# Performance work log

Measured on AMD Instinct MI355X. Metric: run time of the kernel, lower is better.

The kernel has to match this reference:

```python
import jax, jax.numpy as jnp
import numpy as np

D_MODEL = 32
KEY_CH = 32
HEADS = 4
BIAS = 0.1


def setup_inputs() -> dict:
    key = jax.random.key(0)
    ks = jax.random.split(key, 8)
    Nu, Ni, d = 8192, 8192, D_MODEL
    s = 1.0 / np.sqrt(d)
    return {
        "user_embeddings": jax.random.normal(ks[0], (Nu, d), jnp.float32),
        "item_embeddings": jax.random.normal(ks[1], (Ni, d), jnp.float32),
        "keys_w": jax.random.uniform(ks[2], (d, KEY_CH), jnp.float32, -s, s),
        "keys_b": jax.random.uniform(ks[3], (KEY_CH,), jnp.float32, -s, s),
        "queries_w": jax.random.uniform(ks[4], (d, KEY_CH), jnp.float32, -s, s),
        "queries_b": jax.random.uniform(ks[5], (KEY_CH,), jnp.float32, -s, s),
        "reproj_w": jax.random.uniform(ks[6], (KEY_CH * HEADS, KEY_CH), jnp.float32, -s, s),
        "reproj_b": jax.random.uniform(ks[7], (KEY_CH,), jnp.float32, -s, s),
    }


def reference(user_embeddings, item_embeddings, keys_w, keys_b,
              queries_w, queries_b, reproj_w, reproj_b):
    Nu, d = user_embeddings.shape
    Ni = item_embeddings.shape[0]
    hk = KEY_CH // HEADS  # per-head key channels = 8
    keys = user_embeddings @ keys_w + keys_b          # [Nu, 32]
    queries = item_embeddings @ queries_w + queries_b  # [Ni, 32]
    # split into heads: [N, H, hk]
    k = jax.nn.softmax(keys.reshape(Nu, HEADS, hk), axis=0)      # softmax over users (dim 0)
    q = jax.nn.softmax(queries.reshape(Ni, HEADS, hk), axis=2)   # softmax over features (dim 1)
    # context per head: relu(key @ query^T - 0.1) -> [H, Nu, Ni]
    ctx = jax.nn.relu(jnp.einsum('uhk,ihk->hui', k, q) - BIAS)
    # attended = context^T @ user_embeddings -> [Ni, H, d]
    att = jnp.einsum('hui,ud->ihd', ctx, user_embeddings)
    agg = att.reshape(Ni, HEADS * d)  # concat heads along dim 1 (head-major, matches torch.cat)
    proj = agg @ reproj_w + reproj_b  # [Ni, 32]
    # dropout is identity in eval mode; residual add
    return item_embeddings + proj
```

## Files before the change

kernel.cpp:

```cpp
#include <hip/hip_runtime.h>

#define NU 8192
#define NI 8192
#define DM 32
#define KC 32
#define HEADS 4
#define HK 8
#define BIASV 0.1f

#define UBLK 128

__global__ __launch_bounds__(256) void k_embed(
    const float* __restrict__ U, const float* __restrict__ I,
    const float* __restrict__ Wk, const float* __restrict__ bk,
    const float* __restrict__ Wq, const float* __restrict__ bq,
    float* __restrict__ keys, float* __restrict__ q,
    float* __restrict__ part_s, float* __restrict__ part_m)
{
    __shared__ float Ws[DM * KC];
    __shared__ float bs[KC];
    __shared__ float wps[4][HEADS][HK];
    __shared__ float wpm[4][HEADS][HK];

    const int blk = blockIdx.x;
    const int t   = threadIdx.x;
    const int g   = blk * 256 + t;
    const int row = g >> 2;
    const int qr  = g & 3;
    const bool is_user = (row < NU);

    const float* W  = is_user ? Wk : Wq;
    const float* bb = is_user ? bk : bq;
    for (int i = t; i < DM * KC; i += 256) Ws[i] = W[i];
    if (t < KC) bs[t] = bb[t];
    __syncthreads();

    const float* Erow = is_user ? (U + row * DM) : (I + (row - NU) * DM);
    float e[DM];
    const float4* ev = (const float4*)Erow;
    #pragma unroll
    for (int j = 0; j < DM / 4; ++j) {
        float4 v = ev[j];
        e[4*j+0] = v.x; e[4*j+1] = v.y; e[4*j+2] = v.z; e[4*j+3] = v.w;
    }
    float o[HK];
    #pragma unroll
    for (int j = 0; j < HK; ++j) {
        float s = bs[qr * HK + j];
        #pragma unroll
        for (int dd = 0; dd < DM; ++dd) s += e[dd] * Ws[dd * KC + qr * HK + j];
        o[j] = s;
    }

    if (is_user) {
        float4* dst = (float4*)(keys + row * KC + qr * HK);
        dst[0] = make_float4(o[0], o[1], o[2], o[3]);
        dst[1] = make_float4(o[4], o[5], o[6], o[7]);
        float sx[HK], mx[HK];
        #pragma unroll
        for (int j = 0; j < HK; ++j) { sx[j] = __expf(o[j]); mx[j] = o[j]; }
        #pragma unroll
        for (int m = 4; m < 64; m <<= 1) {
            #pragma unroll
            for (int j = 0; j < HK; ++j) {
                sx[j] += __shfl_xor(sx[j], m, 64);
                mx[j]  = fmaxf(mx[j], __shfl_xor(mx[j], m, 64));
            }
        }
        const int lane = t & 63, wv = t >> 6;
        if (lane < 4) {
            #pragma unroll
            for (int j = 0; j < HK; ++j) { wps[wv][lane][j] = sx[j]; wpm[wv][lane][j] = mx[j]; }
        }
        __syncthreads();
        if (t < KC) {
            const int h = t >> 3, j = t & 7;
            part_s[blk * KC + t] = wps[0][h][j] + wps[1][h][j] + wps[2][h][j] + wps[3][h][j];
            part_m[blk * KC + t] = fmaxf(fmaxf(wpm[0][h][j], wpm[1][h][j]),
                                         fmaxf(wpm[2][h][j], wpm[3][h][j]));
        }
    } else {
        float m = o[0];
        #pragma unroll
        for (int j = 1; j < HK; ++j) m = fmaxf(m, o[j]);
        float sum = 0.f;
        #pragma unroll
        for (int j = 0; j < HK; ++j) { float tt = __expf(o[j] - m); o[j] = tt; sum += tt; }
        float inv = 1.f / sum;
        float4* dst = (float4*)(q + (row - NU) * KC + qr * HK);
        dst[0] = make_float4(o[0]*inv, o[1]*inv, o[2]*inv, o[3]*inv);
        dst[1] = make_float4(o[4]*inv, o[5]*inv, o[6]*inv, o[7]*inv);
    }
}

__global__ __launch_bounds__(256) void k_out(
    const float* __restrict__ U, const float* __restrict__ I,
    const float* __restrict__ keys, const float* __restrict__ q,
    const float* __restrict__ Wr, const float* __restrict__ br,
    const float* __restrict__ part_s, const float* __restrict__ part_m,
    float* __restrict__ out)
{
    __shared__ float red_s[8][KC], red_m[8][KC];
    __shared__ float sinv[KC];
    __shared__ int active;

    const int t = threadIdx.x;
    const int c = t & 31, ch = t >> 5;
    if (t == 0) active = 0;
    {
        float s = 0.f, m = -1e30f;
        for (int b = ch; b < UBLK; b += 8) {
            s += part_s[b * KC + c];
            m = fmaxf(m, part_m[b * KC + c]);
        }
        red_s[ch][c] = s; red_m[ch][c] = m;
    }
    __syncthreads();
    if (t < KC) {
        float ss = 0.f, mm = -1e30f;
        #pragma unroll
        for (int i = 0; i < 8; ++i) { ss += red_s[i][t]; mm = fmaxf(mm, red_m[i][t]); }
        const float inv = 1.f / ss;
        sinv[t] = inv;
        if (__expf(mm) * inv > BIASV) active = 1;
    }
    __syncthreads();

    if (!active) {
        const int g = blockIdx.x * 256 + t;
        const float4 brv = ((const float4*)br)[t & 7];
        const float4 iv  = ((const float4*)I)[g];
        ((float4*)out)[g] = make_float4(iv.x + brv.x, iv.y + brv.y,
                                        iv.z + brv.z, iv.w + brv.w);
        return;
    }

    __shared__ float q_s[32][KC];
    __shared__ float k_s[64][KC];
    __shared__ float U_s[64][DM];
    __shared__ float agg[32][HEADS * DM];
    __shared__ float Wr_s[HEADS * DM * KC];

    const int itbase = blockIdx.x * 32;
    for (int i = t; i < 32 * KC; i += 256) q_s[i >> 5][i & 31] = q[itbase * KC + i];
    for (int i = t; i < HEADS * DM * KC; i += 256) Wr_s[i] = Wr[i];

    const int il  = t >> 3;
    const int sub = t & 7;
    float acc[HEADS][4] = {{0.f}};

    for (int cu = 0; cu < NU / 64; ++cu) {
        __syncthreads();
        for (int i = t; i < 64 * KC; i += 256) {
            const int lr = i >> 5, lc = i & 31;
            k_s[lr][lc] = __expf(keys[(cu * 64 + lr) * KC + i % KC]) * sinv[lc];
            U_s[lr][lc] = U[(cu * 64 + lr) * DM + lc];
        }
        __syncthreads();
        for (int lu = 0; lu < 64; ++lu) {
            #pragma unroll
            for (int h = 0; h < HEADS; ++h) {
                float s = 0.f;
                #pragma unroll
                for (int cc = 0; cc < HK; ++cc) s += k_s[lu][h * HK + cc] * q_s[il][h * HK + cc];
                s -= BIASV;
                if (s > 0.f) {
                    #pragma unroll
                    for (int jj = 0; jj < 4; ++jj) acc[h][jj] += s * U_s[lu][sub * 4 + jj];
                }
            }
        }
    }
    #pragma unroll
    for (int h = 0; h < HEADS; ++h)
        #pragma unroll
        for (int jj = 0; jj < 4; ++jj)
            agg[il][h * DM + sub * 4 + jj] = acc[h][jj];
    __syncthreads();

    float r[4];
    #pragma unroll
    for (int cc = 0; cc < 4; ++cc) r[cc] = br[sub * 4 + cc];
    for (int j = 0; j < HEADS * DM; ++j) {
        const float a = agg[il][j];
        #pragma unroll
        for (int cc = 0; cc < 4; ++cc) r[cc] += a * Wr_s[j * KC + sub * 4 + cc];
    }
    #pragma unroll
    for (int cc = 0; cc < 4; ++cc) {
        const int idx = (itbase + il) * KC + sub * 4 + cc;
        out[idx] = I[idx] + r[cc];
    }
}

extern "C" void kernel_launch(void* const* d_in, const int* in_sizes, int n_in,
                              void* d_out, int out_size, void* d_ws, size_t ws_size,
                              hipStream_t stream) {
    const float* U  = (const float*)d_in[0];
    const float* I  = (const float*)d_in[1];
    const float* Wk = (const float*)d_in[2];
    const float* bk = (const float*)d_in[3];
    const float* Wq = (const float*)d_in[4];
    const float* bq = (const float*)d_in[5];
    const float* Wr = (const float*)d_in[6];
    const float* br = (const float*)d_in[7];
    float* out = (float*)d_out;

    float* ws_keys = (float*)d_ws;
    float* ws_q    = ws_keys + NU * KC;
    float* ws_ps   = ws_q + NI * KC;
    float* ws_pm   = ws_ps + UBLK * KC;

    k_embed<<<256, 256, 0, stream>>>(U, I, Wk, bk, Wq, bq, ws_keys, ws_q, ws_ps, ws_pm);
    k_out<<<256, 256, 0, stream>>>(U, I, ws_keys, ws_q, Wr, br, ws_ps, ws_pm, out);
}
```

Before: 15.52 us.

## Recompute key and query projections inside the output kernel, drop intermediate buffers

The first kernel now computes only the user-side key softmax statistics (partial sums and maxima) over 128 blocks. It no longer projects items or writes the full keys and queries arrays to workspace. The output kernel instead recomputes queries for its item tile and keys per 64-user chunk from shared copies of Wk and Wq. The reprojection weights are read from global memory instead of being staged in shared memory. This removes the global write and read of the key and query intermediates and halves the first launch, at the cost of redundant projection arithmetic in every output block whenever the dense path is taken.

```diff
diff --git a/kernel.cpp b/kernel.cpp
--- a/kernel.cpp
+++ b/kernel.cpp
@@ -10,92 +10,65 @@
 
 #define UBLK 128
 
-__global__ __launch_bounds__(256) void k_embed(
-    const float* __restrict__ U, const float* __restrict__ I,
+__global__ __launch_bounds__(256) void k_part(
+    const float* __restrict__ U,
     const float* __restrict__ Wk, const float* __restrict__ bk,
-    const float* __restrict__ Wq, const float* __restrict__ bq,
-    float* __restrict__ keys, float* __restrict__ q,
     float* __restrict__ part_s, float* __restrict__ part_m)
 {
     __shared__ float Ws[DM * KC];
     __shared__ float bs[KC];
-    __shared__ float wps[4][HEADS][HK];
-    __shared__ float wpm[4][HEADS][HK];
-
-    const int blk = blockIdx.x;
-    const int t   = threadIdx.x;
-    const int g   = blk * 256 + t;
-    const int row = g >> 2;
-    const int qr  = g & 3;
-    const bool is_user = (row < NU);
-
-    const float* W  = is_user ? Wk : Wq;
-    const float* bb = is_user ? bk : bq;
-    for (int i = t; i < DM * KC; i += 256) Ws[i] = W[i];
-    if (t < KC) bs[t] = bb[t];
-    __syncthreads();
-
-    const float* Erow = is_user ? (U + row * DM) : (I + (row - NU) * DM);
+    __shared__ float wps[4][KC], wpm[4][KC];
+
+    const int blk = blockIdx.x, t = threadIdx.x;
+    for (int i = t; i < DM * KC; i += 256) Ws[i] = Wk[i];
+    if (t < KC) bs[t] = bk[t];
+    __syncthreads();
+
+    const int row = (blk * 256 + t) >> 2;
+    const int qr  = t & 3;
     float e[DM];
-    const float4* ev = (const float4*)Erow;
+    const float4* ev = (const float4*)(U + row * DM);
     #pragma unroll
     for (int j = 0; j < DM / 4; ++j) {
         float4 v = ev[j];
         e[4*j+0] = v.x; e[4*j+1] = v.y; e[4*j+2] = v.z; e[4*j+3] = v.w;
     }
-    float o[HK];
+    float sx[HK], mx[HK];
     #pragma unroll
     for (int j = 0; j < HK; ++j) {
         float s = bs[qr * HK + j];
         #pragma unroll
-        for (int dd = 0; dd < DM; ++dd) s += e[dd] * Ws[dd * KC + qr * HK + j];
-        o[j] = s;
-    }
-
-    if (is_user) {
-        float4* dst = (float4*)(keys + row * KC + qr * HK);
-        dst[0] = make_float4(o[0], o[1], o[2], o[3]);
-        dst[1] = make_float4(o[4], o[5], o[6], o[7]);
-        float sx[HK], mx[HK];
-        #pragma unroll
-        for (int j = 0; j < HK; ++j) { sx[j] = __expf(o[j]); mx[j] = o[j]; }
-        #pragma unroll
-        for (int m = 4; m < 64; m <<= 1) {
-            #pragma unroll
-            for (int j = 0; j < HK; ++j) {
-                sx[j] += __shfl_xor(sx[j], m, 64);
-                mx[j]  = fmaxf(mx[j], __shfl_xor(mx[j], m, 64));
-            }
-        }
-        const int lane = t & 63, wv = t >> 6;
-        if (lane < 4) {
-            #pragma unroll
-            for (int j = 0; j < HK; ++j) { wps[wv][lane][j] = sx[j]; wpm[wv][lane][j] = mx[j]; }
-        }
-        __syncthreads();
-        if (t < KC) {
-            const int h = t >> 3, j = t & 7;
-            part_s[blk * KC + t] = wps[0][h][j] + wps[1][h][j] + wps[2][h][j] + wps[3][h][j];
-            part_m[blk * KC + t] = fmaxf(fmaxf(wpm[0][h][j], wpm[1][h][j]),
-                                         fmaxf(wpm[2][h][j], wpm[3][h][j]));
-        }
-    } else {
-        float m = o[0];
-        #pragma unroll
-        for (int j = 1; j < HK; ++j) m = fmaxf(m, o[j]);
-        float sum = 0.f;
-        #pragma unroll
-        for (int j = 0; j < HK; ++j) { float tt = __expf(o[j] - m); o[j] = tt; sum += tt; }
-        float inv = 1.f / sum;
-        float4* dst = (float4*)(q + (row - NU) * KC + qr * HK);
-        dst[0] = make_float4(o[0]*inv, o[1]*inv, o[2]*inv, o[3]*inv);
-        dst[1] = make_float4(o[4]*inv, o[5]*inv, o[6]*inv, o[7]*inv);
+        for (int d = 0; d < DM; ++d) s += e[d] * Ws[d * KC + qr * HK + j];
+        mx[j] = s; sx[j] = __expf(s);
+    }
+    #pragma unroll
+    for (int m = 4; m < 64; m <<= 1) {
+        #pragma unroll
+        for (int j = 0; j < HK; ++j) {
+            sx[j] += __shfl_xor(sx[j], m, 64);
+            mx[j]  = fmaxf(mx[j], __shfl_xor(mx[j], m, 64));
+        }
+    }
+    const int lane = t & 63, wv = t >> 6;
+    if (lane < 4) {
+        #pragma unroll
+        for (int j = 0; j < HK; ++j) {
+            wps[wv][lane * HK + j] = sx[j];
+            wpm[wv][lane * HK + j] = mx[j];
+        }
+    }
+    __syncthreads();
+    if (t < KC) {
+        part_s[blk * KC + t] = wps[0][t] + wps[1][t] + wps[2][t] + wps[3][t];
+        part_m[blk * KC + t] = fmaxf(fmaxf(wpm[0][t], wpm[1][t]),
+                                     fmaxf(wpm[2][t], wpm[3][t]));
     }
 }
 
 __global__ __launch_bounds__(256) void k_out(
     const float* __restrict__ U, const float* __restrict__ I,
-    const float* __restrict__ keys, const float* __restrict__ q,
+    const float* __restrict__ Wk, const float* __restrict__ bk,
+    const float* __restrict__ Wq, const float* __restrict__ bq,
     const float* __restrict__ Wr, const float* __restrict__ br,
     const float* __restrict__ part_s, const float* __restrict__ part_m,
     float* __restrict__ out)
@@ -135,15 +108,39 @@
         return;
     }
 
+    __shared__ float Wk_s[DM * KC], Wq_s[DM * KC];
+    __shared__ float bk_s[KC], bq_s[KC];
     __shared__ float q_s[32][KC];
+    __shared__ float U_s[64][DM];
     __shared__ float k_s[64][KC];
-    __shared__ float U_s[64][DM];
     __shared__ float agg[32][HEADS * DM];
-    __shared__ float Wr_s[HEADS * DM * KC];
+
+    for (int i = t; i < DM * KC; i += 256) { Wk_s[i] = Wk[i]; Wq_s[i] = Wq[i]; }
+    if (t < KC) { bk_s[t] = bk[t]; bq_s[t] = bq[t]; }
+    __syncthreads();
 
     const int itbase = blockIdx.x * 32;
-    for (int i = t; i < 32 * KC; i += 256) q_s[i >> 5][i & 31] = q[itbase * KC + i];
-    for (int i = t; i < HEADS * DM * KC; i += 256) Wr_s[i] = Wr[i];
+    if (t < 128) {
+        const int il = t >> 2, h = t & 3;
+        const float* Ir = I + (itbase + il) * DM;
+        float o[HK];
+        #pragma unroll
+        for (int j = 0; j < HK; ++j) {
+            float s2 = bq_s[h * HK + j];
+            #pragma unroll
+            for (int d = 0; d < DM; ++d) s2 += Ir[d] * Wq_s[d * KC + h * HK + j];
+            o[j] = s2;
+        }
+        float mm = o[0];
+        #pragma unroll
+        for (int j = 1; j < HK; ++j) mm = fmaxf(mm, o[j]);
+        float ss = 0.f;
+        #pragma unroll
+        for (int j = 0; j < HK; ++j) { o[j] = __expf(o[j] - mm); ss += o[j]; }
+        const float inv = 1.f / ss;
+        #pragma unroll
+        for (int j = 0; j < HK; ++j) q_s[il][h * HK + j] = o[j] * inv;
+    }
 
     const int il  = t >> 3;
     const int sub = t & 7;
@@ -151,22 +148,33 @@
 
     for (int cu = 0; cu < NU / 64; ++cu) {
         __syncthreads();
-        for (int i = t; i < 64 * KC; i += 256) {
-            const int lr = i >> 5, lc = i & 31;
-            k_s[lr][lc] = __expf(keys[(cu * 64 + lr) * KC + i % KC]) * sinv[lc];
-            U_s[lr][lc] = U[(cu * 64 + lr) * DM + lc];
+        for (int i = t; i < 64 * DM; i += 256) U_s[i >> 5][i & 31] = U[cu * 64 * DM + i];
+        __syncthreads();
+        {
+            const int lu = t >> 2, qh = t & 3;
+            float o[HK];
+            #pragma unroll
+            for (int j = 0; j < HK; ++j) {
+                float s2 = bk_s[qh * HK + j];
+                #pragma unroll
+                for (int d = 0; d < DM; ++d) s2 += U_s[lu][d] * Wk_s[d * KC + qh * HK + j];
+                o[j] = s2;
+            }
+            #pragma unroll
+            for (int j = 0; j < HK; ++j)
+                k_s[lu][qh * HK + j] = __expf(o[j]) * sinv[qh * HK + j];
         }
         __syncthreads();
         for (int lu = 0; lu < 64; ++lu) {
             #pragma unroll
             for (int h = 0; h < HEADS; ++h) {
-                float s = 0.f;
+                float s2 = 0.f;
                 #pragma unroll
-                for (int cc = 0; cc < HK; ++cc) s += k_s[lu][h * HK + cc] * q_s[il][h * HK + cc];
-                s -= BIASV;
-                if (s > 0.f) {
+                for (int cc = 0; cc < HK; ++cc) s2 += k_s[lu][h * HK + cc] * q_s[il][h * HK + cc];
+                s2 -= BIASV;
+                if (s2 > 0.f) {
                     #pragma unroll
-                    for (int jj = 0; jj < 4; ++jj) acc[h][jj] += s * U_s[lu][sub * 4 + jj];
+                    for (int jj = 0; jj < 4; ++jj) acc[h][jj] += s2 * U_s[lu][sub * 4 + jj];
                 }
             }
         }
@@ -184,7 +192,7 @@
     for (int j = 0; j < HEADS * DM; ++j) {
         const float a = agg[il][j];
         #pragma unroll
-        for (int cc = 0; cc < 4; ++cc) r[cc] += a * Wr_s[j * KC + sub * 4 + cc];
+        for (int cc = 0; cc < 4; ++cc) r[cc] += a * Wr[j * KC + sub * 4 + cc];
     }
     #pragma unroll
     for (int cc = 0; cc < 4; ++cc) {
@@ -206,11 +214,9 @@
     const float* br = (const float*)d_in[7];
     float* out = (float*)d_out;
 
-    float* ws_keys = (float*)d_ws;
-    float* ws_q    = ws_keys + NU * KC;
-    float* ws_ps   = ws_q + NI * KC;
-    float* ws_pm   = ws_ps + UBLK * KC;
-
-    k_embed<<<256, 256, 0, stream>>>(U, I, Wk, bk, Wq, bq, ws_keys, ws_q, ws_ps, ws_pm);
-    k_out<<<256, 256, 0, stream>>>(U, I, ws_keys, ws_q, Wr, br, ws_ps, ws_pm, out);
+    float* ws_ps = (float*)d_ws;
+    float* ws_pm = ws_ps + UBLK * KC;
+
+    k_part<<<UBLK, 256, 0, stream>>>(U, Wk, bk, ws_ps, ws_pm);
+    k_out<<<256, 256, 0, stream>>>(U, I, Wk, bk, Wq, bq, Wr, br, ws_ps, ws_pm, out);
 }
```

New measurement: 15.34 us. Within noise of the previous version (-1.2%).
